# Kernel tuning notes

Hardware: AMD Instinct MI355X
Metric: run time of the kernel (lower is better)

## Reference

```python
import jax, jax.numpy as jnp
import numpy as np

B = 16384
MV = 512   # movie_vector_size
UV = 512   # user_vector_size
NM = 16    # num_dense_movie_embeddings
NU = 16    # num_dense_user_embeddings
DS = 16    # dense_embedding_size
MLP = [256, 128, 1]


def setup_inputs() -> dict:
    key = jax.random.key(0)
    ks = jax.random.split(key, 12)
    inp = {
        'movie_vectors': jax.random.normal(ks[0], (B, MV), jnp.float32),
        'user_vectors': jax.random.normal(ks[1], (B, UV), jnp.float32),
        # embedding towers: Linear(in, DS*N + 1), stored as [in, out]
        'Wm': jax.random.normal(ks[2], (MV, DS * NM + 1), jnp.float32) * (1.0 / np.sqrt(MV)),
        'bm': jax.random.normal(ks[3], (DS * NM + 1,), jnp.float32) * 0.01,
        'Wu': jax.random.normal(ks[4], (UV, DS * NU + 1), jnp.float32) * (1.0 / np.sqrt(UV)),
        'bu': jax.random.normal(ks[5], (DS * NU + 1,), jnp.float32) * 0.01,
    }
    d_in = (NM + NU) * DS  # 512
    dims = [d_in] + MLP
    for i in range(len(MLP)):
        inp[f'W{i+1}'] = jax.random.normal(ks[6 + 2*i], (dims[i], dims[i+1]), jnp.float32) * (1.0 / np.sqrt(dims[i]))
        inp[f'b{i+1}'] = jax.random.normal(ks[7 + 2*i], (dims[i+1],), jnp.float32) * 0.01
    return inp


def reference(movie_vectors, user_vectors, Wm, bm, Wu, bu, W1, b1, W2, b2, W3, b3):
    batch = movie_vectors.shape[0]
    movie_dense = movie_vectors @ Wm + bm          # [B, DS*NM+1]
    user_dense = user_vectors @ Wu + bu            # [B, DS*NU+1]
    fm_additive = movie_dense[:, -1] + user_dense[:, -1]            # [B]
    m_split = movie_dense[:, :-1].reshape(batch, NM, DS)            # [B, NM, DS]
    u_split = user_dense[:, :-1].reshape(batch, NU, DS)             # [B, NU, DS]
    fm_interactions = jnp.einsum('bik,bjk->bij', m_split, u_split).reshape(batch, -1)  # [B, NM*NU]
    all_dense = jnp.concatenate([movie_dense[:, :-1], user_dense[:, :-1]], axis=-1)    # [B, (NM+NU)*DS]
    h = jax.nn.relu(all_dense @ W1 + b1)
    h = jax.nn.relu(h @ W2 + b2)
    mlp_out = h @ W3 + b3                                           # [B, 1]
    logit = mlp_out + fm_additive[:, None] + jnp.sum(fm_interactions, axis=-1, keepdims=True)
    return logit
```

## Files before the change

### kernel.cpp

```cpp
#include <hip/hip_runtime.h>


#define NTH 1024
#define RB  64

typedef __bf16 bf16x8 __attribute__((ext_vector_type(8)));
typedef float  f32x4  __attribute__((ext_vector_type(4)));

#define WS_WMF  0
#define WS_WUF  294912
#define WS_W1F  589824
#define WS_W2F  851968
#define WS_BIAS 917504
#define WS_CS   917760

#define BPITCH  528
#define L_BST   0
#define L_DENSE 67584
#define L_FM    133120
#define L_ADD   141824
#define L_OUT   142336
#define LDSB    142592

__device__ __forceinline__ unsigned short f2bf(float f) {
  unsigned u = __builtin_bit_cast(unsigned, f);
  u += 0x7FFFu + ((u >> 16) & 1u);
  return (unsigned short)(u >> 16);
}

__device__ __forceinline__ f32x4 mfma_bf16(bf16x8 a, bf16x8 b, f32x4 c) {
  return __builtin_amdgcn_mfma_f32_16x16x32_bf16(a, b, c, 0, 0, 0);
}

extern "C" __global__ __launch_bounds__(256) void deepfm_colsum(
    const float* __restrict__ Wm, const float* __restrict__ Wu,
    char* __restrict__ ws) {
  const int rid = blockIdx.x * 4 + (threadIdx.x >> 6);
  const int l = threadIdx.x & 63;
  const float* W = (rid >= 512) ? Wu : Wm;
  const int k = rid & 511;
  float4 v = *(const float4*)(W + (size_t)k * 257 + l * 4);
#pragma unroll
  for (int s = 4; s < 64; s <<= 1) {
    v.x += __shfl_xor(v.x, s, 64);
    v.y += __shfl_xor(v.y, s, 64);
    v.z += __shfl_xor(v.z, s, 64);
    v.w += __shfl_xor(v.w, s, 64);
  }
  if (l < 4) {
    float* CS = (float*)(ws + WS_CS);
    CS[rid * 16 + l * 4 + 0] = v.x;
    CS[rid * 16 + l * 4 + 1] = v.y;
    CS[rid * 16 + l * 4 + 2] = v.z;
    CS[rid * 16 + l * 4 + 3] = v.w;
  }
}

extern "C" __global__ __launch_bounds__(256) void deepfm_prep(
    const float* __restrict__ Wm, const float* __restrict__ bm,
    const float* __restrict__ Wu, const float* __restrict__ bu,
    const float* __restrict__ W1, const float* __restrict__ W2,
    const float* __restrict__ b3, char* __restrict__ ws) {
  const int unit = blockIdx.x * 4 + (threadIdx.x >> 6);
  if (unit >= 897) return;
  const int l = threadIdx.x & 63;
  const int fi = l & 15, q = l >> 4;
  unsigned short h[8];
  if (unit < 576) {
    const int t = unit / 288, rem = unit % 288;
    const int kg = rem / 18, ft = rem % 18;
    const float* W = t ? Wu : Wm;
    const float* CS = (const float*)(ws + WS_CS);
    char* outp = ws + (t ? WS_WUF : WS_WMF);
    const int f = ft * 16 + fi;
#pragma unroll
    for (int e = 0; e < 8; ++e) {
      const int k = kg * 32 + q * 8 + e;
      float val;
      if (f < 256) val = W[k * 257 + f];
      else if (f < 272) val = CS[(t * 512 + k) * 16 + (f - 256)];
      else if (f == 272) val = W[k * 257 + 256];
      else val = 0.f;
      h[e] = f2bf(val);
    }
    uint4 o;
    o.x = h[0] | ((unsigned)h[1] << 16); o.y = h[2] | ((unsigned)h[3] << 16);
    o.z = h[4] | ((unsigned)h[5] << 16); o.w = h[6] | ((unsigned)h[7] << 16);
    *(uint4*)(outp + (((kg * 18 + ft) * 64 + l) << 4)) = o;
  } else if (unit < 832) {
    const int bb = unit - 576;
    const int kg = bb / 16, ft = bb % 16;
    const int f = ft * 16 + fi;
#pragma unroll
    for (int e = 0; e < 8; ++e) h[e] = f2bf(W1[(kg * 32 + q * 8 + e) * 256 + f]);
    uint4 o;
    o.x = h[0] | ((unsigned)h[1] << 16); o.y = h[2] | ((unsigned)h[3] << 16);
    o.z = h[4] | ((unsigned)h[5] << 16); o.w = h[6] | ((unsigned)h[7] << 16);
    *(uint4*)(ws + WS_W1F + (((kg * 16 + ft) * 64 + l) << 4)) = o;
  } else if (unit < 896) {
    const int bb = unit - 832;
    const int kg = bb / 8, ft = bb % 8;
    const int f = ft * 16 + fi;
#pragma unroll
    for (int e = 0; e < 8; ++e) h[e] = f2bf(W2[(kg * 32 + q * 8 + e) * 128 + f]);
    uint4 o;
    o.x = h[0] | ((unsigned)h[1] << 16); o.y = h[2] | ((unsigned)h[3] << 16);
    o.z = h[4] | ((unsigned)h[5] << 16); o.w = h[6] | ((unsigned)h[7] << 16);
    *(uint4*)(ws + WS_W2F + (((kg * 8 + ft) * 64 + l) << 4)) = o;
  } else {
    float* aux = (float*)(ws + WS_BIAS);
    if (l < 16) {
      float s = 0.f;
      for (int i = 0; i < 16; ++i) s += bm[i * 16 + l];
      aux[l] = s;
    } else if (l < 32) {
      const int k = l - 16;
      float s = 0.f;
      for (int i = 0; i < 16; ++i) s += bu[i * 16 + k];
      aux[l] = s;
    } else if (l == 32) {
      aux[32] = bm[256] + bu[256] + b3[0];
    }
  }
}

extern "C" __global__ __launch_bounds__(NTH, 4) void deepfm_main(
    const float* __restrict__ movie, const float* __restrict__ user,
    const float* __restrict__ bm, const float* __restrict__ bu,
    const float* __restrict__ b1, const float* __restrict__ b2,
    const float* __restrict__ W3, const char* __restrict__ ws,
    float* __restrict__ out) {
  extern __shared__ __align__(16) char lds[];
  char* const bstage    = lds + L_BST;
  char* const densefrag = lds + L_DENSE;
  char* const h1frag    = lds + L_BST;
  float* const fmbuf    = (float*)(lds + L_FM);
  float* const addbuf   = (float*)(lds + L_ADD);
  float* const outpart  = (float*)(lds + L_OUT);

  const int tid = threadIdx.x;
  const int w   = tid >> 6;
  const int l   = tid & 63;
  const int cn  = l & 15;
  const int q   = l >> 4;
  const int row0 = blockIdx.x * RB;

  const int tw   = w >> 3;
  const int wi   = w & 7;
  const int axi  = wi & 1;
  const int axrt = wi >> 1;

  const f32x4 zz = {0.f, 0.f, 0.f, 0.f};
  const float* auxb = (const float*)(ws + WS_BIAS);

  {
    const char* WF = ws + (tw ? WS_WUF : WS_WMF);
    const char* brow = bstage + tw * 64 * BPITCH;
    f32x4 a0r0 = zz, a0r1 = zz, a0r2 = zz, a0r3 = zz;
    f32x4 a1r0 = zz, a1r1 = zz, a1r2 = zz, a1r3 = zz;
    f32x4 axc = zz;

    for (int h = 0; h < 2; ++h) {
      if (h) __syncthreads();
#pragma unroll
      for (int p = 0; p < 8; ++p) {
        const int idx = p * 1024 + tid;
        const int r = idx >> 6, f4 = idx & 63;
        const float* src = (r >= 64) ? user : movie;
        const float4 v = *(const float4*)(src + (size_t)(row0 + (r & 63)) * 512 +
                                          h * 256 + f4 * 4);
        uint2 o;
        o.x = f2bf(v.x) | ((unsigned)f2bf(v.y) << 16);
        o.y = f2bf(v.z) | ((unsigned)f2bf(v.w) << 16);
        *(uint2*)(bstage + r * BPITCH + f4 * 8) = o;
      }
      __syncthreads();

#pragma unroll 2
      for (int kgl = 0; kgl < 8; ++kgl) {
        const int kg = h * 8 + kgl;
        const bf16x8 bf0 = *(const bf16x8*)(brow + cn * BPITCH + kgl * 64 + q * 16);
        const bf16x8 bf1 = *(const bf16x8*)(brow + (16 + cn) * BPITCH + kgl * 64 + q * 16);
        const bf16x8 bf2 = *(const bf16x8*)(brow + (32 + cn) * BPITCH + kgl * 64 + q * 16);
        const bf16x8 bf3 = *(const bf16x8*)(brow + (48 + cn) * BPITCH + kgl * 64 + q * 16);
        const bf16x8 A0 = *(const bf16x8*)(WF + (((kg * 18 + wi * 2 + 0) * 64 + l) << 4));
        const bf16x8 A1 = *(const bf16x8*)(WF + (((kg * 18 + wi * 2 + 1) * 64 + l) << 4));
        const bf16x8 AX = *(const bf16x8*)(WF + (((kg * 18 + 16 + axi) * 64 + l) << 4));
        a0r0 = mfma_bf16(A0, bf0, a0r0);  a0r1 = mfma_bf16(A0, bf1, a0r1);
        a0r2 = mfma_bf16(A0, bf2, a0r2);  a0r3 = mfma_bf16(A0, bf3, a0r3);
        a1r0 = mfma_bf16(A1, bf0, a1r0);  a1r1 = mfma_bf16(A1, bf1, a1r1);
        a1r2 = mfma_bf16(A1, bf2, a1r2);  a1r3 = mfma_bf16(A1, bf3, a1r3);
        const bf16x8 bsel = (axrt == 0) ? bf0 : (axrt == 1) ? bf1
                          : (axrt == 2) ? bf2 : bf3;
        axc = mfma_bf16(AX, bsel, axc);
      }
    }

    const float* bt = tw ? bu : bm;
    const f32x4 accA[2][4] = {{a0r0, a0r1, a0r2, a0r3}, {a1r0, a1r1, a1r2, a1r3}};
#pragma unroll
    for (int s = 0; s < 2; ++s) {
      const int ft = wi * 2 + s;
      const int fb = ft * 16 + q * 4;
      const float g0 = bt[fb], g1 = bt[fb + 1], g2 = bt[fb + 2], g3 = bt[fb + 3];
      const int kd = tw * 256 + fb;
      const int kgd = kd >> 5, qd = (kd >> 3) & 3, ed = kd & 4;
#pragma unroll
      for (int rt = 0; rt < 4; ++rt) {
        const f32x4 v = accA[s][rt];
        uint2 p;
        p.x = f2bf(v[0] + g0) | ((unsigned)f2bf(v[1] + g1) << 16);
        p.y = f2bf(v[2] + g2) | ((unsigned)f2bf(v[3] + g3) << 16);
        *(uint2*)(densefrag + (((kgd * 4 + rt) * 64 + qd * 16 + cn) << 4) +
                  (ed ? 8 : 0)) = p;
      }
    }

    if (axi == 0) {
#pragma unroll
      for (int reg = 0; reg < 4; ++reg)
        fmbuf[(tw * 64 + axrt * 16 + cn) * 17 + (q * 4 + reg)] = axc[reg];
    } else if (q == 0) {
      addbuf[tw * 64 + axrt * 16 + cn] = axc[0];
    }
  }

  __syncthreads();

  if (tid < 64) {
    float p = 0.f;
#pragma unroll
    for (int k = 0; k < 16; ++k)
      p += (fmbuf[tid * 17 + k] + auxb[k]) *
           (fmbuf[(64 + tid) * 17 + k] + auxb[16 + k]);
    outpart[tid] = p + addbuf[tid] + addbuf[64 + tid] + auxb[32];
  }

  {
    const char* W1F = ws + WS_W1F;
    f32x4 r0 = zz, r1 = zz, r2 = zz, r3 = zz;
#pragma unroll 4
    for (int kg = 0; kg < 16; ++kg) {
      const bf16x8 b0 = *(const bf16x8*)(densefrag + (((kg * 4 + 0) * 64 + l) << 4));
      const bf16x8 b1f = *(const bf16x8*)(densefrag + (((kg * 4 + 1) * 64 + l) << 4));
      const bf16x8 b2f = *(const bf16x8*)(densefrag + (((kg * 4 + 2) * 64 + l) << 4));
      const bf16x8 b3f = *(const bf16x8*)(densefrag + (((kg * 4 + 3) * 64 + l) << 4));
      const bf16x8 a0 = *(const bf16x8*)(W1F + (((kg * 16 + w) * 64 + l) << 4));
      r0 = mfma_bf16(a0, b0,  r0);
      r1 = mfma_bf16(a0, b1f, r1);
      r2 = mfma_bf16(a0, b2f, r2);
      r3 = mfma_bf16(a0, b3f, r3);
    }
    const f32x4 accA[4] = {r0, r1, r2, r3};
    const int fb = w * 16 + q * 4;
    const float g0 = b1[fb], g1 = b1[fb + 1], g2 = b1[fb + 2], g3 = b1[fb + 3];
    const int kgd = fb >> 5, qd = (fb >> 3) & 3, ed = fb & 4;
#pragma unroll
    for (int rt = 0; rt < 4; ++rt) {
      const f32x4 v = accA[rt];
      uint2 p;
      p.x = f2bf(fmaxf(v[0] + g0, 0.f)) | ((unsigned)f2bf(fmaxf(v[1] + g1, 0.f)) << 16);
      p.y = f2bf(fmaxf(v[2] + g2, 0.f)) | ((unsigned)f2bf(fmaxf(v[3] + g3, 0.f)) << 16);
      *(uint2*)(h1frag + (((kgd * 4 + rt) * 64 + qd * 16 + cn) << 4) +
                (ed ? 8 : 0)) = p;
    }
  }

  __syncthreads();

  {
    const char* W2F = ws + WS_W2F;
    const int ftw = w & 7;
    const int rth = w >> 3;
    f32x4 d0 = zz, d1 = zz;
#pragma unroll 4
    for (int kg = 0; kg < 8; ++kg) {
      const bf16x8 b0 = *(const bf16x8*)(h1frag + (((kg * 4 + rth * 2 + 0) * 64 + l) << 4));
      const bf16x8 b1f = *(const bf16x8*)(h1frag + (((kg * 4 + rth * 2 + 1) * 64 + l) << 4));
      const bf16x8 a0 = *(const bf16x8*)(W2F + (((kg * 8 + ftw) * 64 + l) << 4));
      d0 = mfma_bf16(a0, b0,  d0);
      d1 = mfma_bf16(a0, b1f, d1);
    }
    const int fb = ftw * 16 + q * 4;
    float bb[4], ww[4];
#pragma unroll
    for (int i = 0; i < 4; ++i) { bb[i] = b2[fb + i]; ww[i] = W3[fb + i]; }
    const f32x4 acc3[2] = {d0, d1};
#pragma unroll
    for (int j = 0; j < 2; ++j) {
      const int rt = rth * 2 + j;
      float p = 0.f;
#pragma unroll
      for (int reg = 0; reg < 4; ++reg)
        p += fmaxf(acc3[j][reg] + bb[reg], 0.f) * ww[reg];
      p += __shfl_xor(p, 16, 64);
      p += __shfl_xor(p, 32, 64);
      if (l < 16) atomicAdd(&outpart[rt * 16 + cn], p);
    }
  }

  __syncthreads();
  if (tid < 64) out[row0 + tid] = outpart[tid];
}

extern "C" void kernel_launch(void* const* d_in, const int* in_sizes, int n_in,
                              void* d_out, int out_size, void* d_ws, size_t ws_size,
                              hipStream_t stream) {
  const float* movie = (const float*)d_in[0];
  const float* user  = (const float*)d_in[1];
  const float* Wm = (const float*)d_in[2];
  const float* bm = (const float*)d_in[3];
  const float* Wu = (const float*)d_in[4];
  const float* bu = (const float*)d_in[5];
  const float* W1 = (const float*)d_in[6];
  const float* b1 = (const float*)d_in[7];
  const float* W2 = (const float*)d_in[8];
  const float* b2 = (const float*)d_in[9];
  const float* W3 = (const float*)d_in[10];
  const float* b3 = (const float*)d_in[11];
  char* ws = (char*)d_ws;
  float* out = (float*)d_out;

  (void)hipFuncSetAttribute((const void*)deepfm_main,
                            hipFuncAttributeMaxDynamicSharedMemorySize, LDSB);

  deepfm_colsum<<<256, 256, 0, stream>>>(Wm, Wu, ws);
  deepfm_prep<<<225, 256, 0, stream>>>(Wm, bm, Wu, bu, W1, W2, b3, ws);
  deepfm_main<<<256, NTH, LDSB, stream>>>(movie, user, bm, bu, b1, b2, W3, ws, out);
}
```

Before: 131.9 us.

## Fuse weight prep and main kernel via cooperative launch with grid sync

Merges the colsum, prep and main kernels into one cooperative kernel. Each block stages its first half of activations into LDS, does a slice of the weight repacking (computing column sums inline instead of in a separate kernel), then a grid-wide sync precedes the main compute. This removes two kernel launches and their serialization gaps, and overlaps the input loads with the prep work. In exchange it adds grid-barrier cost and redundant column-sum arithmetic per prep unit, and keeps a three-kernel fallback if the cooperative launch fails.

```diff
diff --git a/kernel.cpp b/kernel.cpp
--- a/kernel.cpp
+++ b/kernel.cpp
@@ -1,4 +1,5 @@
 #include <hip/hip_runtime.h>
+#include <hip/hip_cooperative_groups.h>
 
 
 #define NTH 1024
@@ -32,45 +33,17 @@
   return __builtin_amdgcn_mfma_f32_16x16x32_bf16(a, b, c, 0, 0, 0);
 }
 
-extern "C" __global__ __launch_bounds__(256) void deepfm_colsum(
-    const float* __restrict__ Wm, const float* __restrict__ Wu,
-    char* __restrict__ ws) {
-  const int rid = blockIdx.x * 4 + (threadIdx.x >> 6);
-  const int l = threadIdx.x & 63;
-  const float* W = (rid >= 512) ? Wu : Wm;
-  const int k = rid & 511;
-  float4 v = *(const float4*)(W + (size_t)k * 257 + l * 4);
-#pragma unroll
-  for (int s = 4; s < 64; s <<= 1) {
-    v.x += __shfl_xor(v.x, s, 64);
-    v.y += __shfl_xor(v.y, s, 64);
-    v.z += __shfl_xor(v.z, s, 64);
-    v.w += __shfl_xor(v.w, s, 64);
-  }
-  if (l < 4) {
-    float* CS = (float*)(ws + WS_CS);
-    CS[rid * 16 + l * 4 + 0] = v.x;
-    CS[rid * 16 + l * 4 + 1] = v.y;
-    CS[rid * 16 + l * 4 + 2] = v.z;
-    CS[rid * 16 + l * 4 + 3] = v.w;
-  }
-}
-
-extern "C" __global__ __launch_bounds__(256) void deepfm_prep(
-    const float* __restrict__ Wm, const float* __restrict__ bm,
+__device__ __forceinline__ void prep_unit(
+    int unit, int l, const float* __restrict__ Wm, const float* __restrict__ bm,
     const float* __restrict__ Wu, const float* __restrict__ bu,
     const float* __restrict__ W1, const float* __restrict__ W2,
-    const float* __restrict__ b3, char* __restrict__ ws) {
-  const int unit = blockIdx.x * 4 + (threadIdx.x >> 6);
-  if (unit >= 897) return;
-  const int l = threadIdx.x & 63;
+    const float* __restrict__ b3, char* __restrict__ ws, int CSmode) {
   const int fi = l & 15, q = l >> 4;
   unsigned short h[8];
   if (unit < 576) {
     const int t = unit / 288, rem = unit % 288;
     const int kg = rem / 18, ft = rem % 18;
     const float* W = t ? Wu : Wm;
-    const float* CS = (const float*)(ws + WS_CS);
     char* outp = ws + (t ? WS_WUF : WS_WMF);
     const int f = ft * 16 + fi;
 #pragma unroll
@@ -78,8 +51,16 @@
       const int k = kg * 32 + q * 8 + e;
       float val;
       if (f < 256) val = W[k * 257 + f];
-      else if (f < 272) val = CS[(t * 512 + k) * 16 + (f - 256)];
-      else if (f == 272) val = W[k * 257 + 256];
+      else if (f < 272) {
+        if (CSmode) {
+          val = ((const float*)(ws + WS_CS))[(t * 512 + k) * 16 + (f - 256)];
+        } else {
+          float s = 0.f;
+#pragma unroll
+          for (int i = 0; i < 16; ++i) s += W[k * 257 + i * 16 + (f - 256)];
+          val = s;
+        }
+      } else if (f == 272) val = W[k * 257 + 256];
       else val = 0.f;
       h[e] = f2bf(val);
     }
@@ -124,13 +105,12 @@
   }
 }
 
-extern "C" __global__ __launch_bounds__(NTH, 4) void deepfm_main(
+__device__ __forceinline__ void main_body(
     const float* __restrict__ movie, const float* __restrict__ user,
     const float* __restrict__ bm, const float* __restrict__ bu,
     const float* __restrict__ b1, const float* __restrict__ b2,
     const float* __restrict__ W3, const char* __restrict__ ws,
-    float* __restrict__ out) {
-  extern __shared__ __align__(16) char lds[];
+    float* __restrict__ out, char* lds) {
   char* const bstage    = lds + L_BST;
   char* const densefrag = lds + L_DENSE;
   char* const h1frag    = lds + L_BST;
@@ -161,21 +141,22 @@
     f32x4 axc = zz;
 
     for (int h = 0; h < 2; ++h) {
-      if (h) __syncthreads();
-#pragma unroll
-      for (int p = 0; p < 8; ++p) {
-        const int idx = p * 1024 + tid;
-        const int r = idx >> 6, f4 = idx & 63;
-        const float* src = (r >= 64) ? user : movie;
-        const float4 v = *(const float4*)(src + (size_t)(row0 + (r & 63)) * 512 +
-                                          h * 256 + f4 * 4);
-        uint2 o;
-        o.x = f2bf(v.x) | ((unsigned)f2bf(v.y) << 16);
-        o.y = f2bf(v.z) | ((unsigned)f2bf(v.w) << 16);
-        *(uint2*)(bstage + r * BPITCH + f4 * 8) = o;
+      if (h) {
+        __syncthreads();
+#pragma unroll
+        for (int p = 0; p < 8; ++p) {
+          const int idx = p * 1024 + tid;
+          const int r = idx >> 6, f4 = idx & 63;
+          const float* src = (r >= 64) ? user : movie;
+          const float4 v = *(const float4*)(src + (size_t)(row0 + (r & 63)) * 512 +
+                                            256 + f4 * 4);
+          uint2 o;
+          o.x = f2bf(v.x) | ((unsigned)f2bf(v.y) << 16);
+          o.y = f2bf(v.z) | ((unsigned)f2bf(v.w) << 16);
+          *(uint2*)(bstage + r * BPITCH + f4 * 8) = o;
+        }
+        __syncthreads();
       }
-      __syncthreads();
-
 #pragma unroll 2
       for (int kgl = 0; kgl < 8; ++kgl) {
         const int kg = h * 8 + kgl;
@@ -303,6 +284,103 @@
   if (tid < 64) out[row0 + tid] = outpart[tid];
 }
 
+extern "C" __global__ __launch_bounds__(NTH, 4) void deepfm_fused(
+    const float* __restrict__ movie, const float* __restrict__ user,
+    const float* __restrict__ Wm, const float* __restrict__ bm,
+    const float* __restrict__ Wu, const float* __restrict__ bu,
+    const float* __restrict__ W1, const float* __restrict__ b1,
+    const float* __restrict__ W2, const float* __restrict__ b2,
+    const float* __restrict__ W3, const float* __restrict__ b3,
+    char* __restrict__ ws, float* __restrict__ out) {
+  extern __shared__ __align__(16) char lds[];
+  char* const bstage = lds + L_BST;
+
+  const int tid = threadIdx.x;
+  const int w   = tid >> 6;
+  const int l   = tid & 63;
+  const int row0 = blockIdx.x * RB;
+
+#pragma unroll
+  for (int p = 0; p < 8; ++p) {
+    const int idx = p * 1024 + tid;
+    const int r = idx >> 6, f4 = idx & 63;
+    const float* src = (r >= 64) ? user : movie;
+    const float4 v = *(const float4*)(src + (size_t)(row0 + (r & 63)) * 512 + f4 * 4);
+    uint2 o;
+    o.x = f2bf(v.x) | ((unsigned)f2bf(v.y) << 16);
+    o.y = f2bf(v.z) | ((unsigned)f2bf(v.w) << 16);
+    *(uint2*)(bstage + r * BPITCH + f4 * 8) = o;
+  }
+
+  const int unit = blockIdx.x * 16 + w;
+  if (unit < 897)
+    prep_unit(unit, l, Wm, bm, Wu, bu, W1, W2, b3, ws, 0);
+
+  __threadfence();
+  cooperative_groups::this_grid().sync();
+
+  main_body(movie, user, bm, bu, b1, b2, W3, ws, out, lds);
+}
+
+extern "C" __global__ __launch_bounds__(256) void deepfm_colsum(
+    const float* __restrict__ Wm, const float* __restrict__ Wu,
+    char* __restrict__ ws) {
+  const int rid = blockIdx.x * 4 + (threadIdx.x >> 6);
+  const int l = threadIdx.x & 63;
+  const float* W = (rid >= 512) ? Wu : Wm;
+  const int k = rid & 511;
+  float4 v = *(const float4*)(W + (size_t)k * 257 + l * 4);
+#pragma unroll
+  for (int s = 4; s < 64; s <<= 1) {
+    v.x += __shfl_xor(v.x, s, 64);
+    v.y += __shfl_xor(v.y, s, 64);
+    v.z += __shfl_xor(v.z, s, 64);
+    v.w += __shfl_xor(v.w, s, 64);
+  }
+  if (l < 4) {
+    float* CS = (float*)(ws + WS_CS);
+    CS[rid * 16 + l * 4 + 0] = v.x;
+    CS[rid * 16 + l * 4 + 1] = v.y;
+    CS[rid * 16 + l * 4 + 2] = v.z;
+    CS[rid * 16 + l * 4 + 3] = v.w;
+  }
+}
+
+extern "C" __global__ __launch_bounds__(256) void deepfm_prep(
+    const float* __restrict__ Wm, const float* __restrict__ bm,
+    const float* __restrict__ Wu, const float* __restrict__ bu,
+    const float* __restrict__ W1, const float* __restrict__ W2,
+    const float* __restrict__ b3, char* __restrict__ ws) {
+  const int unit = blockIdx.x * 4 + (threadIdx.x >> 6);
+  if (unit >= 897) return;
+  prep_unit(unit, threadIdx.x & 63, Wm, bm, Wu, bu, W1, W2, b3, ws, 1);
+}
+
+extern "C" __global__ __launch_bounds__(NTH, 4) void deepfm_main(
+    const float* __restrict__ movie, const float* __restrict__ user,
+    const float* __restrict__ bm, const float* __restrict__ bu,
+    const float* __restrict__ b1, const float* __restrict__ b2,
+    const float* __restrict__ W3, const char* __restrict__ ws,
+    float* __restrict__ out) {
+  extern __shared__ __align__(16) char lds[];
+  char* const bstage = lds + L_BST;
+  const int tid = threadIdx.x;
+  const int row0 = blockIdx.x * RB;
+#pragma unroll
+  for (int p = 0; p < 8; ++p) {
+    const int idx = p * 1024 + tid;
+    const int r = idx >> 6, f4 = idx & 63;
+    const float* src = (r >= 64) ? user : movie;
+    const float4 v = *(const float4*)(src + (size_t)(row0 + (r & 63)) * 512 + f4 * 4);
+    uint2 o;
+    o.x = f2bf(v.x) | ((unsigned)f2bf(v.y) << 16);
+    o.y = f2bf(v.z) | ((unsigned)f2bf(v.w) << 16);
+    *(uint2*)(bstage + r * BPITCH + f4 * 8) = o;
+  }
+  __syncthreads();
+  main_body(movie, user, bm, bu, b1, b2, W3, ws, out, lds);
+}
+
 extern "C" void kernel_launch(void* const* d_in, const int* in_sizes, int n_in,
                               void* d_out, int out_size, void* d_ws, size_t ws_size,
                               hipStream_t stream) {
@@ -321,10 +399,21 @@
   char* ws = (char*)d_ws;
   float* out = (float*)d_out;
 
+  (void)hipFuncSetAttribute((const void*)deepfm_fused,
+                            hipFuncAttributeMaxDynamicSharedMemorySize, LDSB);
   (void)hipFuncSetAttribute((const void*)deepfm_main,
                             hipFuncAttributeMaxDynamicSharedMemorySize, LDSB);
 
-  deepfm_colsum<<<256, 256, 0, stream>>>(Wm, Wu, ws);
-  deepfm_prep<<<225, 256, 0, stream>>>(Wm, bm, Wu, bu, W1, W2, b3, ws);
-  deepfm_main<<<256, NTH, LDSB, stream>>>(movie, user, bm, bu, b1, b2, W3, ws, out);
-}
+  void* kargs[] = {(void*)&movie, (void*)&user, (void*)&Wm, (void*)&bm,
+                   (void*)&Wu, (void*)&bu, (void*)&W1, (void*)&b1,
+                   (void*)&W2, (void*)&b2, (void*)&W3, (void*)&b3,
+                   (void*)&ws, (void*)&out};
+  hipError_t err = hipLaunchCooperativeKernel((const void*)deepfm_fused,
+                                              dim3(256), dim3(NTH), kargs,
+                                              LDSB, stream);
+  if (err != hipSuccess) {
+    deepfm_colsum<<<256, 256, 0, stream>>>(Wm, Wu, ws);
+    deepfm_prep<<<225, 256, 0, stream>>>(Wm, bm, Wu, bu, W1, W2, b3, ws);
+    deepfm_main<<<256, NTH, LDSB, stream>>>(movie, user, bm, bu, b1, b2, W3, ws, out);
+  }
+}
```

New measurement: 273.0 us. +106.9%, slower.
